# Kernel tuning notes

Measured on AMD Instinct MI355X. Metric: run time of the kernel, lower is better.

Reference implementation:

```python
import jax, jax.numpy as jnp
import numpy as np

B, S, HID, NH = 2, 2048, 1024, 16
HD = HID // NH  # head_dim = 64


def setup_inputs() -> dict:
    key = jax.random.key(0)
    ks = jax.random.split(key, 5)
    sc = 1.0 / np.sqrt(HID)
    return {
        "x":  jax.random.normal(ks[0], (B, S, HID), dtype=jnp.float32),
        "Wq": jax.random.normal(ks[1], (HID, HID), dtype=jnp.float32) * sc,
        "bq": jax.random.normal(ks[2], (HID,), dtype=jnp.float32) * 0.01,
        "Wo": jax.random.normal(ks[3], (HID, HID), dtype=jnp.float32) * sc,
        "bo": jax.random.normal(ks[4], (HID,), dtype=jnp.float32) * 0.01,
    }


def reference(x, Wq, bq, Wo, bo):
    Bv, Sv, _ = x.shape
    # NOTE: source module (faithfully) uses self.q projection for q, k AND v.
    q = (x @ Wq + bq).reshape(Bv, Sv, NH, HD).transpose(0, 2, 1, 3)  # [B,H,S,D]
    k = q
    v = q
    # NOTE: source uses floor division `//` by sqrt(head_dim) -- reproduced.
    scale = jnp.asarray(HD, x.dtype) ** 0.5
    scores = jnp.floor(jnp.einsum("bhqd,bhkd->bhqk", q, k) / scale)  # [B,H,S,S]
    attn = jax.nn.softmax(scores, axis=-1)
    out = jnp.einsum("bhqk,bhkd->bhqd", attn, v)  # [B,H,S,D]
    out = out.transpose(0, 2, 1, 3).reshape(Bv, Sv, HID)
    return out @ Wo + bo
```

## Files before the change

### kernel.cpp

```cpp
#include <hip/hip_runtime.h>
#include <math.h>

#define BB 2
#define SS 2048
#define HIDD 1024
#define NHH 16
#define HDD 64

using f4 = __attribute__((ext_vector_type(4))) float;

template<int OUT_MODE>
__global__ __launch_bounds__(256)
void gemm_kernel(const float* __restrict__ A, const float* __restrict__ W,
                 const float* __restrict__ bias, float* __restrict__ C)
{
    constexpr int M = BB * SS, N = HIDD, K = HIDD;
    constexpr int BM = 128, BN = 64, BK = 16, NK = K / BK;
    constexpr int LDA = 132, LDW = 68;
    __shared__ float As[2][BK][LDA];
    __shared__ float Ws[2][BK][LDW];

    const int tid = threadIdx.x;
    const int tx = tid & 15, ty = tid >> 4;

    const int swz = (blockIdx.x & 7) * 64 + (blockIdx.x >> 3);
    const int n0 = (swz & 15) * BN;
    const int m0 = (swz >> 4) * BM;

    const int a_m = tid >> 2;
    const int a_k = (tid & 3) * 4;
    const int w_k = tid >> 4;
    const int w_n = (tid & 15) * 4;

    const float* Abase = A + (size_t)m0 * K;
    const float* Wbase = W + n0;

    f4 pa0, pa1, pw0;

#define G_LOAD(kt) {                                                        \
    const float* Ap = Abase + (size_t)(kt) * BK + a_k;                      \
    pa0 = *(const f4*)(Ap + (size_t)a_m * K);                               \
    pa1 = *(const f4*)(Ap + (size_t)(a_m + 64) * K);                        \
    pw0 = *(const f4*)(Wbase + (size_t)((kt) * BK + w_k) * N + w_n); }

#define LDS_WRITE(buf) {                                                    \
    As[buf][a_k+0][a_m]      = pa0[0]; As[buf][a_k+1][a_m]      = pa0[1];   \
    As[buf][a_k+2][a_m]      = pa0[2]; As[buf][a_k+3][a_m]      = pa0[3];   \
    As[buf][a_k+0][a_m+64]   = pa1[0]; As[buf][a_k+1][a_m+64]   = pa1[1];   \
    As[buf][a_k+2][a_m+64]   = pa1[2]; As[buf][a_k+3][a_m+64]   = pa1[3];   \
    *(f4*)&Ws[buf][w_k][w_n] = pw0; }

    float acc[8][4] = {};

    G_LOAD(0);
    LDS_WRITE(0);
    __syncthreads();

    int cur = 0;
    for (int kt = 0; kt < NK; ++kt) {
        if (kt + 1 < NK) G_LOAD(kt + 1);
        #pragma unroll 4
        for (int k = 0; k < BK; ++k) {
            f4 af0 = *(const f4*)&As[cur][k][4 * ty];
            f4 af1 = *(const f4*)&As[cur][k][64 + 4 * ty];
            f4 bf  = *(const f4*)&Ws[cur][k][4 * tx];
            #pragma unroll
            for (int i = 0; i < 4; ++i) {
                #pragma unroll
                for (int j = 0; j < 4; ++j) {
                    acc[i][j]     = fmaf(af0[i], bf[j], acc[i][j]);
                    acc[i+4][j]   = fmaf(af1[i], bf[j], acc[i+4][j]);
                }
            }
        }
        if (kt + 1 < NK) LDS_WRITE(cur ^ 1);
        __syncthreads();
        cur ^= 1;
    }

    f4 biasv = *(const f4*)&bias[n0 + 4 * tx];
    #pragma unroll
    for (int i = 0; i < 8; ++i) {
        const int m = m0 + 4 * ty + ((i < 4) ? i : (64 + i - 4));
        f4 v;
        #pragma unroll
        for (int j = 0; j < 4; ++j) v[j] = acc[i][j] + biasv[j];
        if (OUT_MODE == 0) {
            *(f4*)(C + (size_t)m * N + n0 + 4 * tx) = v;
        } else {
            const int b = m >> 11, s = m & (SS - 1);
            const int na = n0 + 4 * tx;
            float* da = C + ((size_t)(b * NHH + (na >> 6)) * SS + s) * HDD + (na & 63);
            *(f4*)da = v;
        }
    }
#undef G_LOAD
#undef LDS_WRITE
}

__global__ __launch_bounds__(256)
void attn_kernel(const float* __restrict__ q, float* __restrict__ o)
{
    constexpr int TS = 64;
    __shared__ float q_s[TS * 64];
    __shared__ float k_s[TS * 64];
    __shared__ float k_t[64][TS];
    __shared__ float P_s[TS][TS];

    const int tid = threadIdx.x;
    const int tx = tid & 15, ty = tid >> 4;

    const int swzb = (blockIdx.x & 7) * 128 + (blockIdx.x >> 3);
    const int qb = swzb & 31;
    const int bh = swzb >> 5;

    #define SWZ(r, w) (((r) << 6) + (((w) ^ ((r) & 15)) << 2))

    const float* qhead = q + (size_t)bh * SS * 64;

    const int st_r = tid >> 2;
    const int st_w = (tid & 3) * 4;

    {
        const float* src = qhead + (size_t)(qb * TS + st_r) * 64 + st_w * 4;
        #pragma unroll
        for (int i = 0; i < 4; ++i) {
            f4 vq = *(const f4*)(src + 4 * i);
            #pragma unroll
            for (int j = 0; j < 4; ++j) vq[j] *= 0.125f;
            *(f4*)&q_s[SWZ(st_r, st_w + i)] = vq;
        }
    }

    float acc_o[4][4] = {};
    float m_r[4] = {-1e30f, -1e30f, -1e30f, -1e30f};
    float l_r[4] = {};

    f4 pk[4];
    {
        const float* src = qhead + (size_t)st_r * 64 + st_w * 4;
        #pragma unroll
        for (int i = 0; i < 4; ++i) pk[i] = *(const f4*)(src + 4 * i);
    }

    for (int kt = 0; kt < SS / TS; ++kt) {
        __syncthreads();
        #pragma unroll
        for (int i = 0; i < 4; ++i) {
            *(f4*)&k_s[SWZ(st_r, st_w + i)] = pk[i];
            const int d = (st_w + i) * 4;
            k_t[d + 0][st_r] = pk[i][0];
            k_t[d + 1][st_r] = pk[i][1];
            k_t[d + 2][st_r] = pk[i][2];
            k_t[d + 3][st_r] = pk[i][3];
        }
        __syncthreads();
        if (kt + 1 < SS / TS) {
            const float* src = qhead + (size_t)((kt + 1) * TS + st_r) * 64 + st_w * 4;
            #pragma unroll
            for (int i = 0; i < 4; ++i) pk[i] = *(const f4*)(src + 4 * i);
        }

        float sc[4][4] = {};
        #pragma unroll 2
        for (int w = 0; w < 16; ++w) {
            f4 qf[4], kf[4];
            #pragma unroll
            for (int i = 0; i < 4; ++i) qf[i] = *(const f4*)&q_s[SWZ(4 * ty + i, w)];
            #pragma unroll
            for (int l = 0; l < 4; ++l) kf[l] = *(const f4*)&k_t[4 * w + l][4 * tx];
            #pragma unroll
            for (int l = 0; l < 4; ++l)
                #pragma unroll
                for (int i = 0; i < 4; ++i)
                    #pragma unroll
                    for (int j = 0; j < 4; ++j)
                        sc[i][j] = fmaf(qf[i][l], kf[l][j], sc[i][j]);
        }

        #pragma unroll
        for (int i = 0; i < 4; ++i) {
            #pragma unroll
            for (int j = 0; j < 4; ++j)
                sc[i][j] = floorf(sc[i][j]);
            float mx = fmaxf(fmaxf(sc[i][0], sc[i][1]), fmaxf(sc[i][2], sc[i][3]));
            #pragma unroll
            for (int w = 1; w < 16; w <<= 1)
                mx = fmaxf(mx, __shfl_xor(mx, w, 16));
            const float mn = fmaxf(m_r[i], mx);
            const float corr = __expf(m_r[i] - mn);
            m_r[i] = mn;
            f4 p;
            float sum = 0.f;
            #pragma unroll
            for (int j = 0; j < 4; ++j) { p[j] = __expf(sc[i][j] - mn); sum += p[j]; }
            #pragma unroll
            for (int w = 1; w < 16; w <<= 1)
                sum += __shfl_xor(sum, w, 16);
            l_r[i] = l_r[i] * corr + sum;
            #pragma unroll
            for (int j = 0; j < 4; ++j) acc_o[i][j] *= corr;
            *(f4*)&P_s[4 * ty + i][4 * tx] = p;
        }
        __syncthreads();

        #pragma unroll 2
        for (int c = 0; c < TS; c += 4) {
            f4 pf[4], vf[4];
            #pragma unroll
            for (int i = 0; i < 4; ++i) pf[i] = *(const f4*)&P_s[4 * ty + i][c];
            #pragma unroll
            for (int l = 0; l < 4; ++l) vf[l] = *(const f4*)&k_s[SWZ(c + l, tx)];
            #pragma unroll
            for (int l = 0; l < 4; ++l)
                #pragma unroll
                for (int i = 0; i < 4; ++i)
                    #pragma unroll
                    for (int j = 0; j < 4; ++j)
                        acc_o[i][j] = fmaf(pf[i][l], vf[l][j], acc_o[i][j]);
        }
    }

    const int b = bh >> 4, h = bh & 15;
    #pragma unroll
    for (int i = 0; i < 4; ++i) {
        const float inv = 1.0f / l_r[i];
        f4 v;
        #pragma unroll
        for (int j = 0; j < 4; ++j) v[j] = acc_o[i][j] * inv;
        const int srow = qb * TS + 4 * ty + i;
        *(f4*)(o + ((size_t)(b * SS + srow)) * HIDD + h * HDD + 4 * tx) = v;
    }
    #undef SWZ
}

extern "C" void kernel_launch(void* const* d_in, const int* in_sizes, int n_in,
                              void* d_out, int out_size, void* d_ws, size_t ws_size,
                              hipStream_t stream)
{
    const float* x  = (const float*)d_in[0];
    const float* Wq = (const float*)d_in[1];
    const float* bq = (const float*)d_in[2];
    const float* Wo = (const float*)d_in[3];
    const float* bo = (const float*)d_in[4];
    float* out = (float*)d_out;

    float* q_ws    = (float*)d_ws;
    float* attn_ws = q_ws + (size_t)BB * SS * HIDD;

    gemm_kernel<1><<<512, 256, 0, stream>>>(x, Wq, bq, q_ws);
    attn_kernel<<<1024, 256, 0, stream>>>(q_ws, attn_ws);
    gemm_kernel<0><<<512, 256, 0, stream>>>(attn_ws, Wo, bo, out);
}
```

Before: 843.4 us.

## Run attention PV product on bf16x3 MFMA and keep scaled Q in registers

The P·V half of the attention kernel now runs on 16x16x32 bf16 MFMA instructions. P and V are each split into hi/lo bf16 parts and combined over three MFMA passes to keep close to fp32 accuracy. The pre-scaled Q tile moves from LDS into per-thread registers, which removes the Q LDS reads in the QK loop. The barrier between writing P and reading it is dropped, since each wave only reads its own rows. QK^T stays in fp32 because of the floor, and the large Q register array may lower occupancy or cause spills.

```diff
diff --git a/kernel.cpp b/kernel.cpp
--- a/kernel.cpp
+++ b/kernel.cpp
@@ -8,6 +8,18 @@
 #define HDD 64
 
 using f4 = __attribute__((ext_vector_type(4))) float;
+using short8 = __attribute__((ext_vector_type(8))) short;
+using uint2v = __attribute__((ext_vector_type(2))) unsigned int;
+
+__device__ inline unsigned short bf16_rne(float x) {
+    unsigned u = __builtin_bit_cast(unsigned, x);
+    u += 0x7FFFu + ((u >> 16) & 1u);
+    return (unsigned short)(u >> 16);
+}
+__device__ inline float bf16_tof(unsigned short h) {
+    unsigned u = ((unsigned)h) << 16;
+    return __builtin_bit_cast(float, u);
+}
 
 template<int OUT_MODE>
 __global__ __launch_bounds__(256)
@@ -68,8 +80,8 @@
             for (int i = 0; i < 4; ++i) {
                 #pragma unroll
                 for (int j = 0; j < 4; ++j) {
-                    acc[i][j]     = fmaf(af0[i], bf[j], acc[i][j]);
-                    acc[i+4][j]   = fmaf(af1[i], bf[j], acc[i+4][j]);
+                    acc[i][j]   = fmaf(af0[i], bf[j], acc[i][j]);
+                    acc[i+4][j] = fmaf(af1[i], bf[j], acc[i+4][j]);
                 }
             }
         }
@@ -101,38 +113,42 @@
 __global__ __launch_bounds__(256)
 void attn_kernel(const float* __restrict__ q, float* __restrict__ o)
 {
-    constexpr int TS = 64;
-    __shared__ float q_s[TS * 64];
-    __shared__ float k_s[TS * 64];
-    __shared__ float k_t[64][TS];
-    __shared__ float P_s[TS][TS];
+    __shared__ float k_t[64][68];
+    __shared__ unsigned short P_hi[64][72];
+    __shared__ unsigned short P_lo[64][72];
+    __shared__ unsigned short Vt_hi[64][72];
+    __shared__ unsigned short Vt_lo[64][72];
 
     const int tid = threadIdx.x;
     const int tx = tid & 15, ty = tid >> 4;
+    const int lane = tid & 63;
+    const int wv = tid >> 6;
+    const int lr = lane & 15, lh = lane >> 4;
 
     const int swzb = (blockIdx.x & 7) * 128 + (blockIdx.x >> 3);
     const int qb = swzb & 31;
     const int bh = swzb >> 5;
 
-    #define SWZ(r, w) (((r) << 6) + (((w) ^ ((r) & 15)) << 2))
-
     const float* qhead = q + (size_t)bh * SS * 64;
 
     const int st_r = tid >> 2;
     const int st_w = (tid & 3) * 4;
 
+    f4 qreg[4][16];
     {
-        const float* src = qhead + (size_t)(qb * TS + st_r) * 64 + st_w * 4;
-        #pragma unroll
-        for (int i = 0; i < 4; ++i) {
-            f4 vq = *(const f4*)(src + 4 * i);
-            #pragma unroll
-            for (int j = 0; j < 4; ++j) vq[j] *= 0.125f;
-            *(f4*)&q_s[SWZ(st_r, st_w + i)] = vq;
-        }
-    }
-
-    float acc_o[4][4] = {};
+        const float* src = qhead + (size_t)(qb * 64 + 4 * ty) * 64;
+        #pragma unroll
+        for (int i = 0; i < 4; ++i)
+            #pragma unroll
+            for (int w = 0; w < 16; ++w) {
+                f4 vq = *(const f4*)(src + (size_t)i * 64 + 4 * w);
+                #pragma unroll
+                for (int j = 0; j < 4; ++j) vq[j] *= 0.125f;
+                qreg[i][w] = vq;
+            }
+    }
+
+    f4 acc[4] = {};
     float m_r[4] = {-1e30f, -1e30f, -1e30f, -1e30f};
     float l_r[4] = {};
 
@@ -143,30 +159,31 @@
         for (int i = 0; i < 4; ++i) pk[i] = *(const f4*)(src + 4 * i);
     }
 
-    for (int kt = 0; kt < SS / TS; ++kt) {
+    for (int kt = 0; kt < SS / 64; ++kt) {
         __syncthreads();
         #pragma unroll
         for (int i = 0; i < 4; ++i) {
-            *(f4*)&k_s[SWZ(st_r, st_w + i)] = pk[i];
-            const int d = (st_w + i) * 4;
-            k_t[d + 0][st_r] = pk[i][0];
-            k_t[d + 1][st_r] = pk[i][1];
-            k_t[d + 2][st_r] = pk[i][2];
-            k_t[d + 3][st_r] = pk[i][3];
+            #pragma unroll
+            for (int j = 0; j < 4; ++j) {
+                const int d = (st_w + i) * 4 + j;
+                const float v = pk[i][j];
+                k_t[d][st_r] = v;
+                const unsigned short h = bf16_rne(v);
+                Vt_hi[d][st_r] = h;
+                Vt_lo[d][st_r] = bf16_rne(v - bf16_tof(h));
+            }
         }
         __syncthreads();
-        if (kt + 1 < SS / TS) {
-            const float* src = qhead + (size_t)((kt + 1) * TS + st_r) * 64 + st_w * 4;
+        if (kt + 1 < SS / 64) {
+            const float* src = qhead + (size_t)((kt + 1) * 64 + st_r) * 64 + st_w * 4;
             #pragma unroll
             for (int i = 0; i < 4; ++i) pk[i] = *(const f4*)(src + 4 * i);
         }
 
         float sc[4][4] = {};
-        #pragma unroll 2
+        #pragma unroll
         for (int w = 0; w < 16; ++w) {
-            f4 qf[4], kf[4];
-            #pragma unroll
-            for (int i = 0; i < 4; ++i) qf[i] = *(const f4*)&q_s[SWZ(4 * ty + i, w)];
+            f4 kf[4];
             #pragma unroll
             for (int l = 0; l < 4; ++l) kf[l] = *(const f4*)&k_t[4 * w + l][4 * tx];
             #pragma unroll
@@ -175,49 +192,59 @@
                 for (int i = 0; i < 4; ++i)
                     #pragma unroll
                     for (int j = 0; j < 4; ++j)
-                        sc[i][j] = fmaf(qf[i][l], kf[l][j], sc[i][j]);
+                        sc[i][j] = fmaf(qreg[i][w][l], kf[l][j], sc[i][j]);
         }
 
         #pragma unroll
         for (int i = 0; i < 4; ++i) {
             #pragma unroll
-            for (int j = 0; j < 4; ++j)
-                sc[i][j] = floorf(sc[i][j]);
+            for (int j = 0; j < 4; ++j) sc[i][j] = floorf(sc[i][j]);
             float mx = fmaxf(fmaxf(sc[i][0], sc[i][1]), fmaxf(sc[i][2], sc[i][3]));
             #pragma unroll
-            for (int w = 1; w < 16; w <<= 1)
-                mx = fmaxf(mx, __shfl_xor(mx, w, 16));
+            for (int s = 1; s < 16; s <<= 1) mx = fmaxf(mx, __shfl_xor(mx, s, 16));
             const float mn = fmaxf(m_r[i], mx);
             const float corr = __expf(m_r[i] - mn);
             m_r[i] = mn;
-            f4 p;
-            float sum = 0.f;
+            float p[4], sum = 0.f;
             #pragma unroll
             for (int j = 0; j < 4; ++j) { p[j] = __expf(sc[i][j] - mn); sum += p[j]; }
             #pragma unroll
-            for (int w = 1; w < 16; w <<= 1)
-                sum += __shfl_xor(sum, w, 16);
+            for (int s = 1; s < 16; s <<= 1) sum += __shfl_xor(sum, s, 16);
             l_r[i] = l_r[i] * corr + sum;
-            #pragma unroll
-            for (int j = 0; j < 4; ++j) acc_o[i][j] *= corr;
-            *(f4*)&P_s[4 * ty + i][4 * tx] = p;
-        }
-        __syncthreads();
-
-        #pragma unroll 2
-        for (int c = 0; c < TS; c += 4) {
-            f4 pf[4], vf[4];
-            #pragma unroll
-            for (int i = 0; i < 4; ++i) pf[i] = *(const f4*)&P_s[4 * ty + i][c];
-            #pragma unroll
-            for (int l = 0; l < 4; ++l) vf[l] = *(const f4*)&k_s[SWZ(c + l, tx)];
-            #pragma unroll
-            for (int l = 0; l < 4; ++l)
-                #pragma unroll
-                for (int i = 0; i < 4; ++i)
-                    #pragma unroll
-                    for (int j = 0; j < 4; ++j)
-                        acc_o[i][j] = fmaf(pf[i][l], vf[l][j], acc_o[i][j]);
+            acc[0][i] *= corr; acc[1][i] *= corr; acc[2][i] *= corr; acc[3][i] *= corr;
+            unsigned short h0 = bf16_rne(p[0]), h1 = bf16_rne(p[1]);
+            unsigned short h2 = bf16_rne(p[2]), h3 = bf16_rne(p[3]);
+            uint2v uh, ul;
+            uh[0] = (unsigned)h0 | ((unsigned)h1 << 16);
+            uh[1] = (unsigned)h2 | ((unsigned)h3 << 16);
+            unsigned short g0 = bf16_rne(p[0] - bf16_tof(h0));
+            unsigned short g1 = bf16_rne(p[1] - bf16_tof(h1));
+            unsigned short g2 = bf16_rne(p[2] - bf16_tof(h2));
+            unsigned short g3 = bf16_rne(p[3] - bf16_tof(h3));
+            ul[0] = (unsigned)g0 | ((unsigned)g1 << 16);
+            ul[1] = (unsigned)g2 | ((unsigned)g3 << 16);
+            *(uint2v*)&P_hi[4 * ty + i][4 * tx] = uh;
+            *(uint2v*)&P_lo[4 * ty + i][4 * tx] = ul;
+        }
+
+        const int prow = 16 * wv + lr;
+        short8 ah0 = *(const short8*)&P_hi[prow][lh * 8];
+        short8 ah1 = *(const short8*)&P_hi[prow][32 + lh * 8];
+        short8 al0 = *(const short8*)&P_lo[prow][lh * 8];
+        short8 al1 = *(const short8*)&P_lo[prow][32 + lh * 8];
+        #pragma unroll
+        for (int ct = 0; ct < 4; ++ct) {
+            const int vr = 16 * ct + lr;
+            short8 bh0 = *(const short8*)&Vt_hi[vr][lh * 8];
+            short8 bh1 = *(const short8*)&Vt_hi[vr][32 + lh * 8];
+            short8 bl0 = *(const short8*)&Vt_lo[vr][lh * 8];
+            short8 bl1 = *(const short8*)&Vt_lo[vr][32 + lh * 8];
+            acc[ct] = __builtin_amdgcn_mfma_f32_16x16x32_bf16(ah0, bh0, acc[ct], 0, 0, 0);
+            acc[ct] = __builtin_amdgcn_mfma_f32_16x16x32_bf16(al0, bh0, acc[ct], 0, 0, 0);
+            acc[ct] = __builtin_amdgcn_mfma_f32_16x16x32_bf16(ah0, bl0, acc[ct], 0, 0, 0);
+            acc[ct] = __builtin_amdgcn_mfma_f32_16x16x32_bf16(ah1, bh1, acc[ct], 0, 0, 0);
+            acc[ct] = __builtin_amdgcn_mfma_f32_16x16x32_bf16(al1, bh1, acc[ct], 0, 0, 0);
+            acc[ct] = __builtin_amdgcn_mfma_f32_16x16x32_bf16(ah1, bl1, acc[ct], 0, 0, 0);
         }
     }
 
@@ -225,13 +252,12 @@
     #pragma unroll
     for (int i = 0; i < 4; ++i) {
         const float inv = 1.0f / l_r[i];
-        f4 v;
-        #pragma unroll
-        for (int j = 0; j < 4; ++j) v[j] = acc_o[i][j] * inv;
-        const int srow = qb * TS + 4 * ty + i;
-        *(f4*)(o + ((size_t)(b * SS + srow)) * HIDD + h * HDD + 4 * tx) = v;
-    }
-    #undef SWZ
+        const int srow = qb * 64 + 4 * ty + i;
+        float* orow = o + ((size_t)(b * SS + srow)) * HIDD + h * 64;
+        #pragma unroll
+        for (int ct = 0; ct < 4; ++ct)
+            orow[16 * ct + lr] = acc[ct][i] * inv;
+    }
 }
 
 extern "C" void kernel_launch(void* const* d_in, const int* in_sizes, int n_in,
```

Result: slower. 1.148 ms (+36.1%).
